# Kernel tuning notes

Hardware: AMD Instinct MI355X
Metric: run time of the kernel (lower is better)

## Reference

```python
import jax, jax.numpy as jnp
import numpy as np

LN_EPS = 1e-5

def layer_norm(x, g, b):
    mu = jnp.mean(x, axis=-1, keepdims=True)
    var = jnp.mean(jnp.square(x - mu), axis=-1, keepdims=True)
    return (x - mu) * jax.lax.rsqrt(var + LN_EPS) * g + b

def ternary_quant(w):
    # BitNet b1.58-style ternary quantization with straight-through estimator
    scale = 1.0 / jnp.clip(jnp.mean(jnp.abs(w)), 1e-5)
    wq = jnp.clip(jnp.round(w * scale), -1.0, 1.0) / scale
    return w + jax.lax.stop_gradient(wq - w)

def setup_inputs() -> dict:
    key = jax.random.key(0)
    ks = jax.random.split(key, 3)
    dim, hidden = 1024, 4096
    B, S = 8, 1024
    x = jax.random.normal(ks[0], (B, S, dim), dtype=jnp.float32)
    w1 = jax.random.normal(ks[1], (hidden, dim), dtype=jnp.float32) * 0.02
    w2 = jax.random.normal(ks[2], (dim, hidden), dtype=jnp.float32) * 0.02
    return {
        "x": x,
        "ln1_g": jnp.ones((dim,), jnp.float32), "ln1_b": jnp.zeros((dim,), jnp.float32),
        "w1": w1, "b1": jnp.zeros((hidden,), jnp.float32),
        "ln2_g": jnp.ones((hidden,), jnp.float32), "ln2_b": jnp.zeros((hidden,), jnp.float32),
        "w2": w2, "b2": jnp.zeros((dim,), jnp.float32),
    }

def reference(x, ln1_g, ln1_b, w1, b1, ln2_g, ln2_b, w2, b2):
    h = layer_norm(x, ln1_g, ln1_b)
    h = jnp.einsum('bsd,hd->bsh', h, ternary_quant(w1)) + b1  # [B,S,hidden]
    h = jax.nn.gelu(h, approximate=False)  # nn.GELU default is exact erf
    h = layer_norm(h, ln2_g, ln2_b)
    out = jnp.einsum('bsh,dh->bsd', h, ternary_quant(w2)) + b2  # [B,S,dim]
    return out
```

## Files before the change

### kernel.cpp

```cpp
#include <hip/hip_runtime.h>
#include <cstdint>
#include <cstddef>

#define DIM   1024
#define HID   4096
#define MROWS 8192

typedef __attribute__((ext_vector_type(8))) __bf16 bf16x8;
typedef __attribute__((ext_vector_type(4))) float  f32x4;
typedef __attribute__((ext_vector_type(4))) int    i32x4;

__device__ __forceinline__ unsigned short f2bf(float f) {
  unsigned int u = __float_as_uint(f);
  u += 0x7fffu + ((u >> 16) & 1u);
  return (unsigned short)(u >> 16);
}
__device__ __forceinline__ float bf2f(unsigned int lo16) {
  return __uint_as_float(lo16 << 16);
}

__device__ __forceinline__ float fast_gelu(float v) {
  float u = v * (0.79788456080286536f + 0.035677408136300125f * v * v);
  float e = __builtin_amdgcn_exp2f(u * 2.8853900817779268f);
  float r = __builtin_amdgcn_rcpf(e + 1.0f);
  return v - v * r;
}

__device__ __forceinline__ void gld16(const void* g, void* l) {
  auto* gp = reinterpret_cast<__attribute__((address_space(1))) unsigned int*>(
      reinterpret_cast<uintptr_t>(g));
  auto* lp = reinterpret_cast<__attribute__((address_space(3))) unsigned int*>(
      reinterpret_cast<uintptr_t>(l));
  __builtin_amdgcn_global_load_lds(gp, lp, 16, 0, 0);
}

__device__ __forceinline__ void wave_reduce2(float& a, float& b) {
#pragma unroll
  for (int off = 32; off > 0; off >>= 1) {
    a += __shfl_xor(a, off, 64);
    b += __shfl_xor(b, off, 64);
  }
}
__device__ __forceinline__ float wave_reduce_max(float m) {
#pragma unroll
  for (int off = 32; off > 0; off >>= 1) m = fmaxf(m, __shfl_xor(m, off, 64));
  return m;
}

__device__ __forceinline__ void block_reduce2(float& a, float& b, int tid) {
  __shared__ float red[8];
  __syncthreads();
  wave_reduce2(a, b);
  if ((tid & 63) == 0) { red[tid >> 6] = a; red[4 + (tid >> 6)] = b; }
  __syncthreads();
  a = red[0] + red[1] + red[2] + red[3];
  b = red[4] + red[5] + red[6] + red[7];
}

__global__ __launch_bounds__(256)
void prep_kernel(const float* __restrict__ w1, const float* __restrict__ w2,
                 float* __restrict__ part,
                 const float* __restrict__ x, const float* __restrict__ g,
                 const float* __restrict__ b, unsigned int* __restrict__ xn8,
                 float* __restrict__ invs) {
  int tid = threadIdx.x;
  int bid = blockIdx.x;
  if (bid < 2048) {
    const float* w = (bid < 1024) ? w1 : w2;
    int blk = bid & 1023;
    const float4* base = (const float4*)w + (size_t)blk * 1024;
    float s = 0.f;
#pragma unroll
    for (int i = 0; i < 4; ++i) {
      float4 v = base[tid + i * 256];
      s += fabsf(v.x) + fabsf(v.y) + fabsf(v.z) + fabsf(v.w);
    }
#pragma unroll
    for (int off = 32; off > 0; off >>= 1) s += __shfl_xor(s, off, 64);
    __shared__ float red[4];
    if ((tid & 63) == 0) red[tid >> 6] = s;
    __syncthreads();
    if (tid == 0) part[bid] = red[0] + red[1] + red[2] + red[3];
  } else {
    const int row  = (bid - 2048) * 4 + (tid >> 6);
    const int lane = tid & 63;
    const float4* xr = (const float4*)(x + (size_t)row * DIM);
    const float4* g4 = (const float4*)g;
    const float4* b4 = (const float4*)b;
    float4 v[4];
    float s = 0.f, ss = 0.f;
#pragma unroll
    for (int p = 0; p < 4; ++p) {
      v[p] = xr[lane + 64 * p];
      s  += v[p].x + v[p].y + v[p].z + v[p].w;
      ss += v[p].x * v[p].x + v[p].y * v[p].y + v[p].z * v[p].z + v[p].w * v[p].w;
    }
    wave_reduce2(s, ss);
    float mu  = s * (1.0f / DIM);
    float var = ss * (1.0f / DIM) - mu * mu;
    float rs  = rsqrtf(var + 1e-5f);
    float n[4][4];
    float amax = 0.f;
#pragma unroll
    for (int p = 0; p < 4; ++p) {
      float4 gg = g4[lane + 64 * p];
      float4 bb = b4[lane + 64 * p];
      n[p][0] = (v[p].x - mu) * rs * gg.x + bb.x;
      n[p][1] = (v[p].y - mu) * rs * gg.y + bb.y;
      n[p][2] = (v[p].z - mu) * rs * gg.z + bb.z;
      n[p][3] = (v[p].w - mu) * rs * gg.w + bb.w;
#pragma unroll
      for (int c = 0; c < 4; ++c) amax = fmaxf(amax, fabsf(n[p][c]));
    }
    amax = wave_reduce_max(amax);
    float sc, iv;
    if (amax < 1e-20f) { sc = 0.f; iv = 0.f; }
    else               { sc = 127.0f / amax; iv = amax * (1.0f / 127.0f); }
    if (lane == 0) invs[row] = iv;
    unsigned int* dst = xn8 + (size_t)row * 256;
#pragma unroll
    for (int p = 0; p < 4; ++p) {
      unsigned r = 0;
#pragma unroll
      for (int c = 0; c < 4; ++c) {
        int q = (int)rintf(n[p][c] * sc);
        r |= ((unsigned)q & 0xffu) << (8 * c);
      }
      dst[lane + 64 * p] = r;
    }
  }
}

__global__ __launch_bounds__(256)
void quant_kernel(const float* __restrict__ part,
                  const float* __restrict__ w1, unsigned int* __restrict__ q1,
                  const float* __restrict__ w2, unsigned short* __restrict__ q2,
                  const float* __restrict__ g2, const float* __restrict__ b2,
                  const float* __restrict__ bias2,
                  float* __restrict__ Sg, float* __restrict__ Cb,
                  float* __restrict__ scal) {
  int bid = blockIdx.x, tid = threadIdx.x;
  const int lane = tid & 63;
  const float4* psrc = (const float4*)(part + ((bid < 512) ? 0 : 1024));
  float a = 0.f, dummy = 0.f;
#pragma unroll
  for (int p = 0; p < 4; ++p) {
    float4 pv = psrc[lane + 64 * p];
    a += pv.x + pv.y + pv.z + pv.w;
  }
  wave_reduce2(a, dummy);
  float mean = fmaxf(a * (1.0f / 4194304.0f), 1e-5f);
  float sc = 1.0f / mean;

  if (bid < 512) {
    if (bid == 0 && tid == 0) scal[0] = mean;
    const int n4 = 1048576;
    int i = bid * 256 + tid;
    for (; i < n4; i += 512 * 256) {
      float4 v = ((const float4*)w1)[i];
      int t0 = (int)fminf(fmaxf(rintf(v.x * sc), -1.f), 1.f);
      int t1 = (int)fminf(fmaxf(rintf(v.y * sc), -1.f), 1.f);
      int t2 = (int)fminf(fmaxf(rintf(v.z * sc), -1.f), 1.f);
      int t3 = (int)fminf(fmaxf(rintf(v.w * sc), -1.f), 1.f);
      unsigned r = ((unsigned)t0 & 0xffu) | (((unsigned)t1 & 0xffu) << 8) |
                   (((unsigned)t2 & 0xffu) << 16) | (((unsigned)t3 & 0xffu) << 24);
      q1[i] = r;
    }
  } else {
    const int d = bid - 512;
    if (d == 0 && tid == 0) scal[1] = mean;
    const float4* wr = (const float4*)(w2 + (size_t)d * HID);
    const float4* g4 = (const float4*)g2;
    const float4* b4 = (const float4*)b2;
    uint2* qr = (uint2*)(q2 + (size_t)d * HID);
    float s1 = 0.f, s2 = 0.f;
#pragma unroll
    for (int i = 0; i < 4; ++i) {
      int idx = tid + 256 * i;
      float4 wv = wr[idx], gv = g4[idx], bv = b4[idx];
      float t0 = fminf(fmaxf(rintf(wv.x * sc), -1.f), 1.f);
      float t1 = fminf(fmaxf(rintf(wv.y * sc), -1.f), 1.f);
      float t2 = fminf(fmaxf(rintf(wv.z * sc), -1.f), 1.f);
      float t3 = fminf(fmaxf(rintf(wv.w * sc), -1.f), 1.f);
      s1 += gv.x * t0 + gv.y * t1 + gv.z * t2 + gv.w * t3;
      s2 += bv.x * t0 + bv.y * t1 + bv.z * t2 + bv.w * t3;
      uint2 r;
      r.x = (unsigned)f2bf(t0 * gv.x) | ((unsigned)f2bf(t1 * gv.y) << 16);
      r.y = (unsigned)f2bf(t2 * gv.z) | ((unsigned)f2bf(t3 * gv.w) << 16);
      qr[idx] = r;
    }
    block_reduce2(s1, s2, tid);
    if (tid == 0) {
      Sg[d] = mean * s1;
      Cb[d] = mean * s2 + bias2[d];
    }
  }
}

__global__ __launch_bounds__(256)
void gemm1_i8(const unsigned char* __restrict__ A,
              const unsigned char* __restrict__ B,
              unsigned short* __restrict__ H,
              const float* __restrict__ wscale_ptr,
              const float* __restrict__ invs,
              const float* __restrict__ bias,
              float2* __restrict__ sbuf2) {
  __shared__ unsigned char sA[3][128 * 64];
  __shared__ unsigned char sB[3][128 * 64];

  const int tid  = threadIdx.x;
  const int lane = tid & 63;
  const int wave = tid >> 6;
  const int wm   = wave & 1;
  const int wn   = wave >> 1;

  const int nbx  = gridDim.x;
  const int id   = blockIdx.y * nbx + blockIdx.x;
  const int xcd  = id & 7;
  const int slot = id >> 3;
  const int bandsPerXcd = gridDim.y >> 3;
  const int band = xcd * bandsPerXcd + slot / nbx;
  const int col  = slot - (slot / nbx) * nbx;
  const int bm   = band * 128;
  const int bn   = col * 128;

  const int csw = ((tid & 3) ^ ((tid >> 3) & 3)) * 16;
  const unsigned char* Ab = A + (size_t)(bm + (tid >> 2)) * 1024 + csw;
  const unsigned char* Bb = B + (size_t)(bn + (tid >> 2)) * 1024 + csw;

  i32x4 acc[4][4] = {};

  const int rowA = (wm * 64 + (lane & 15)) * 64;
  const int rowB = (wn * 64 + (lane & 15)) * 64;
  const int kc = (((lane >> 4) ^ ((lane >> 1) & 3))) * 16;

  gld16(Ab,                  (char*)&sA[0][0] + tid * 16);
  gld16(Ab + 64 * 1024,      (char*)&sA[0][0] + 4096 + tid * 16);
  gld16(Bb,                  (char*)&sB[0][0] + tid * 16);
  gld16(Bb + 64 * 1024,      (char*)&sB[0][0] + 4096 + tid * 16);
  gld16(Ab + 64,             (char*)&sA[1][0] + tid * 16);
  gld16(Ab + 64 * 1024 + 64, (char*)&sA[1][0] + 4096 + tid * 16);
  gld16(Bb + 64,             (char*)&sB[1][0] + tid * 16);
  gld16(Bb + 64 * 1024 + 64, (char*)&sB[1][0] + 4096 + tid * 16);
  asm volatile("s_waitcnt vmcnt(4)" ::: "memory");
  __builtin_amdgcn_s_barrier();

  int cur = 0, nx2 = 2;
  for (int t = 0; t < 16; ++t) {
    const size_t kn = (t + 2 < 16) ? (size_t)(t + 2) * 64 : 0;
    char* la = (char*)&sA[0][0] + nx2 * 8192;
    char* lb = (char*)&sB[0][0] + nx2 * 8192;
    gld16(Ab + kn,             la + tid * 16);
    gld16(Ab + 64 * 1024 + kn, la + 4096 + tid * 16);
    gld16(Bb + kn,             lb + tid * 16);
    gld16(Bb + 64 * 1024 + kn, lb + 4096 + tid * 16);
    const unsigned char* a = &sA[0][0] + cur * 8192;
    const unsigned char* b = &sB[0][0] + cur * 8192;
    i32x4 af[4], bfr[4];
#pragma unroll
    for (int i = 0; i < 4; ++i) af[i]  = *(const i32x4*)(a + rowA + i * 1024 + kc);
#pragma unroll
    for (int j = 0; j < 4; ++j) bfr[j] = *(const i32x4*)(b + rowB + j * 1024 + kc);
    __builtin_amdgcn_s_setprio(1);
#pragma unroll
    for (int i = 0; i < 4; ++i)
#pragma unroll
      for (int j = 0; j < 4; ++j)
        acc[i][j] = __builtin_amdgcn_mfma_i32_16x16x64_i8(af[i], bfr[j], acc[i][j], 0, 0, 0);
    __builtin_amdgcn_s_setprio(0);
    asm volatile("s_waitcnt vmcnt(4)" ::: "memory");
    __builtin_amdgcn_s_barrier();
    cur = (cur == 2) ? 0 : cur + 1;
    nx2 = (nx2 == 2) ? 0 : nx2 + 1;
  }
  asm volatile("s_waitcnt vmcnt(0)" ::: "memory");

  const float wscale = *wscale_ptr;
  float bv[4];
#pragma unroll
  for (int j = 0; j < 4; ++j) bv[j] = bias[bn + wn * 64 + j * 16 + (lane & 15)];
#pragma unroll
  for (int i = 0; i < 4; ++i) {
    const int m0 = bm + wm * 64 + i * 16 + ((lane >> 4) << 2);
    float asc[4];
#pragma unroll
    for (int r = 0; r < 4; ++r) asc[r] = wscale * invs[m0 + r];
#pragma unroll
    for (int r = 0; r < 4; ++r) {
      float s = 0.f, ss = 0.f;
#pragma unroll
      for (int j = 0; j < 4; ++j) {
        const int n = bn + wn * 64 + j * 16 + (lane & 15);
        float v = fast_gelu((float)acc[i][j][r] * asc[r] + bv[j]);
        H[(size_t)(m0 + r) * HID + n] = f2bf(v);
        s += v; ss += v * v;
      }
#pragma unroll
      for (int off = 1; off < 16; off <<= 1) {
        s  += __shfl_xor(s, off, 64);
        ss += __shfl_xor(ss, off, 64);
      }
      if ((lane & 15) == 0) {
        sbuf2[((size_t)(m0 + r) << 6) + (col << 1) + wn] = make_float2(s, ss);
      }
    }
  }
}

__global__ __launch_bounds__(256)
void murs_fin(const float2* __restrict__ sbuf2, const float* __restrict__ meanp,
              float2* __restrict__ murs) {
  const int row  = blockIdx.x * 4 + (threadIdx.x >> 6);
  const int lane = threadIdx.x & 63;
  float2 v = sbuf2[((size_t)row << 6) + lane];
  float s = v.x, ss = v.y;
  wave_reduce2(s, ss);
  if (lane == 0) {
    float mu  = s * (1.0f / HID);
    float var = ss * (1.0f / HID) - mu * mu;
    float rs  = rsqrtf(var + 1e-5f);
    murs[row] = make_float2(rs * meanp[1], -rs * mu);
  }
}

__global__ __launch_bounds__(512, 2)
void gemm2_v5(const unsigned short* __restrict__ A,
              const unsigned short* __restrict__ B,
              float* __restrict__ C,
              const float2* __restrict__ murs,
              const float* __restrict__ Sg,
              const float* __restrict__ Cb) {
  __shared__ unsigned short sA[3][256 * 64];
  __shared__ unsigned short sB[3][128 * 64];

  const int tid  = threadIdx.x;
  const int lane = tid & 63;
  const int wave = tid >> 6;
  const int wm   = wave >> 1;
  const int wn   = wave & 1;

  const int id   = blockIdx.y * 8 + blockIdx.x;
  const int xcd  = id & 7;
  const int slot = id >> 3;
  const int band = xcd * 4 + (slot >> 3);
  const int col  = slot & 7;
  const int bm   = band * 256;
  const int bn   = col * 128;

  const int csw = ((tid & 7) ^ ((tid >> 3) & 7)) << 3;
  const unsigned short* Ab = A + (size_t)(bm + (tid >> 3)) * 4096 + csw;
  const unsigned short* Bb = B + (size_t)(bn + (tid >> 3)) * 4096 + csw;

  const int rowAb = (wm * 64 + (lane & 15)) * 128;
  const int rowBb = (wn * 64 + (lane & 15)) * 128;
  const int hi    = lane >> 4;
  const int ck0   = ((hi)     ^ (lane & 7)) << 4;
  const int ck1   = ((hi + 4) ^ (lane & 7)) << 4;

  f32x4 acc[4][4] = {};

#pragma unroll
  for (int i = 0; i < 4; ++i) gld16(Ab + (size_t)i * 262144,      (char*)&sA[0][0] + i * 8192 + tid * 16);
#pragma unroll
  for (int i = 0; i < 2; ++i) gld16(Bb + (size_t)i * 262144,      (char*)&sB[0][0] + i * 8192 + tid * 16);
#pragma unroll
  for (int i = 0; i < 4; ++i) gld16(Ab + (size_t)i * 262144 + 64, (char*)&sA[1][0] + i * 8192 + tid * 16);
#pragma unroll
  for (int i = 0; i < 2; ++i) gld16(Bb + (size_t)i * 262144 + 64, (char*)&sB[1][0] + i * 8192 + tid * 16);
  asm volatile("s_waitcnt vmcnt(6)" ::: "memory");
  __builtin_amdgcn_s_barrier();

  int cur = 0, nx2 = 2;
  for (int t = 0; t < 64; ++t) {
    const size_t kn = (t + 2 < 64) ? (size_t)(t + 2) * 64 : 0;
    char* la = (char*)&sA[0][0] + nx2 * 32768;
    char* lb = (char*)&sB[0][0] + nx2 * 16384;
#pragma unroll
    for (int i = 0; i < 4; ++i) gld16(Ab + (size_t)i * 262144 + kn, la + i * 8192 + tid * 16);
#pragma unroll
    for (int i = 0; i < 2; ++i) gld16(Bb + (size_t)i * 262144 + kn, lb + i * 8192 + tid * 16);
    const char* a = (const char*)&sA[0][0] + cur * 32768;
    const char* b = (const char*)&sB[0][0] + cur * 16384;
    bf16x8 af[4][2], bfr[4][2];
#pragma unroll
    for (int i = 0; i < 4; ++i) {
      af[i][0] = *(const bf16x8*)(a + rowAb + i * 2048 + ck0);
      af[i][1] = *(const bf16x8*)(a + rowAb + i * 2048 + ck1);
    }
#pragma unroll
    for (int j = 0; j < 4; ++j) {
      bfr[j][0] = *(const bf16x8*)(b + rowBb + j * 2048 + ck0);
      bfr[j][1] = *(const bf16x8*)(b + rowBb + j * 2048 + ck1);
    }
    __builtin_amdgcn_s_setprio(1);
#pragma unroll
    for (int i = 0; i < 4; ++i)
#pragma unroll
      for (int j = 0; j < 4; ++j)
        acc[i][j] = __builtin_amdgcn_mfma_f32_16x16x32_bf16(af[i][0], bfr[j][0], acc[i][j], 0, 0, 0);
#pragma unroll
    for (int i = 0; i < 4; ++i)
#pragma unroll
      for (int j = 0; j < 4; ++j)
        acc[i][j] = __builtin_amdgcn_mfma_f32_16x16x32_bf16(af[i][1], bfr[j][1], acc[i][j], 0, 0, 0);
    __builtin_amdgcn_s_setprio(0);
    asm volatile("s_waitcnt vmcnt(6)" ::: "memory");
    __builtin_amdgcn_s_barrier();
    cur = (cur == 2) ? 0 : cur + 1;
    nx2 = (nx2 == 2) ? 0 : nx2 + 1;
  }
  asm volatile("s_waitcnt vmcnt(0)" ::: "memory");

  float sg[4], cb[4];
#pragma unroll
  for (int j = 0; j < 4; ++j) {
    const int n = bn + wn * 64 + j * 16 + (lane & 15);
    sg[j] = Sg[n];
    cb[j] = Cb[n];
  }
#pragma unroll
  for (int i = 0; i < 4; ++i) {
    const int m0 = bm + wm * 64 + i * 16 + (hi << 2);
#pragma unroll
    for (int r = 0; r < 4; ++r) {
      float2 ab = murs[m0 + r];
#pragma unroll
      for (int j = 0; j < 4; ++j) {
        const int n = bn + wn * 64 + j * 16 + (lane & 15);
        C[(size_t)(m0 + r) * 1024 + n] = ab.x * acc[i][j][r] + ab.y * sg[j] + cb[j];
      }
    }
  }
}

extern "C" void kernel_launch(void* const* d_in, const int* in_sizes, int n_in,
                              void* d_out, int out_size, void* d_ws, size_t ws_size,
                              hipStream_t stream) {
  const float* x     = (const float*)d_in[0];
  const float* g1    = (const float*)d_in[1];
  const float* b1v   = (const float*)d_in[2];
  const float* w1    = (const float*)d_in[3];
  const float* bias1 = (const float*)d_in[4];
  const float* g2    = (const float*)d_in[5];
  const float* b2v   = (const float*)d_in[6];
  const float* w2    = (const float*)d_in[7];
  const float* bias2 = (const float*)d_in[8];
  float* out = (float*)d_out;

  char* ws = (char*)d_ws;
  float* scal          = (float*)ws;
  float* part          = (float*)(ws + 64);
  float* invs          = (float*)(ws + 16384);
  unsigned int* q1     = (unsigned int*)(ws + 65536);
  unsigned short* q2   = (unsigned short*)(ws + 65536 + 4194304);
  unsigned int* xn8    = (unsigned int*)((char*)q2 + 8388608);
  unsigned short* h    = (unsigned short*)((char*)xn8 + 8388608);
  float2* murs         = (float2*)((char*)h + 67108864);
  float* Sg            = (float*)(murs + 8192);
  float* Cb            = Sg + 1024;
  float2* sbuf2        = (float2*)(Cb + 1024);

  prep_kernel<<<4096, 256, 0, stream>>>(w1, w2, part, x, g1, b1v, xn8, invs);
  quant_kernel<<<1536, 256, 0, stream>>>(part, w1, q1, w2, q2, g2, b2v, bias2, Sg, Cb, scal);
  gemm1_i8<<<dim3(HID / 128, MROWS / 128), 256, 0, stream>>>(
      (const unsigned char*)xn8, (const unsigned char*)q1, h, scal + 0, invs, bias1, sbuf2);
  murs_fin<<<MROWS / 4, 256, 0, stream>>>(sbuf2, scal, murs);
  gemm2_v5<<<dim3(8, 32), 512, 0, stream>>>(h, q2, out, murs, Sg, Cb);
}
```

Measured before the change: 242.5 us.

## Quantize GELU output to int8 per 64-wide segment and run GEMM2 on int8 MFMA

The first GEMM's epilogue now folds ln2 gamma into the GELU output, quantizes it to int8 with a per-row, per-64-column absmax scale, and stores those scales. The second weight is stored as packed ternary int8, using a K ordering that matches the packed activations. GEMM2 becomes an int8 MFMA kernel that rescales each 64-wide K-tile partial into float accumulators. This halves the bytes of the hidden activation written and read, and uses the faster int8 matrix path. In exchange it adds per-tile convert and FMA work in the inner loop, and activation quantization error that could affect accuracy.

```diff
diff --git a/kernel.cpp b/kernel.cpp
--- a/kernel.cpp
+++ b/kernel.cpp
@@ -14,9 +14,6 @@
   unsigned int u = __float_as_uint(f);
   u += 0x7fffu + ((u >> 16) & 1u);
   return (unsigned short)(u >> 16);
-}
-__device__ __forceinline__ float bf2f(unsigned int lo16) {
-  return __uint_as_float(lo16 << 16);
 }
 
 __device__ __forceinline__ float fast_gelu(float v) {
@@ -134,7 +131,7 @@
 __global__ __launch_bounds__(256)
 void quant_kernel(const float* __restrict__ part,
                   const float* __restrict__ w1, unsigned int* __restrict__ q1,
-                  const float* __restrict__ w2, unsigned short* __restrict__ q2,
+                  const float* __restrict__ w2, unsigned int* __restrict__ q2t,
                   const float* __restrict__ g2, const float* __restrict__ b2,
                   const float* __restrict__ bias2,
                   float* __restrict__ Sg, float* __restrict__ Cb,
@@ -169,25 +166,22 @@
   } else {
     const int d = bid - 512;
     if (d == 0 && tid == 0) scal[1] = mean;
-    const float4* wr = (const float4*)(w2 + (size_t)d * HID);
-    const float4* g4 = (const float4*)g2;
-    const float4* b4 = (const float4*)b2;
-    uint2* qr = (uint2*)(q2 + (size_t)d * HID);
+    const float* wr = w2 + (size_t)d * HID;
     float s1 = 0.f, s2 = 0.f;
 #pragma unroll
     for (int i = 0; i < 4; ++i) {
-      int idx = tid + 256 * i;
-      float4 wv = wr[idx], gv = g4[idx], bv = b4[idx];
-      float t0 = fminf(fmaxf(rintf(wv.x * sc), -1.f), 1.f);
-      float t1 = fminf(fmaxf(rintf(wv.y * sc), -1.f), 1.f);
-      float t2 = fminf(fmaxf(rintf(wv.z * sc), -1.f), 1.f);
-      float t3 = fminf(fmaxf(rintf(wv.w * sc), -1.f), 1.f);
-      s1 += gv.x * t0 + gv.y * t1 + gv.z * t2 + gv.w * t3;
-      s2 += bv.x * t0 + bv.y * t1 + bv.z * t2 + bv.w * t3;
-      uint2 r;
-      r.x = (unsigned)f2bf(t0 * gv.x) | ((unsigned)f2bf(t1 * gv.y) << 16);
-      r.y = (unsigned)f2bf(t2 * gv.z) | ((unsigned)f2bf(t3 * gv.w) << 16);
-      qr[idx] = r;
+      const int p32 = tid + 256 * i;
+      const int kb  = (p32 >> 4) * 64 + (p32 & 15);
+      unsigned r = 0;
+#pragma unroll
+      for (int j = 0; j < 4; ++j) {
+        const int k = kb + j * 16;
+        float t = fminf(fmaxf(rintf(wr[k] * sc), -1.f), 1.f);
+        s1 += g2[k] * t;
+        s2 += b2[k] * t;
+        r |= ((unsigned)(int)t & 0xffu) << (8 * j);
+      }
+      q2t[(size_t)d * 1024 + p32] = r;
     }
     block_reduce2(s1, s2, tid);
     if (tid == 0) {
@@ -200,10 +194,12 @@
 __global__ __launch_bounds__(256)
 void gemm1_i8(const unsigned char* __restrict__ A,
               const unsigned char* __restrict__ B,
-              unsigned short* __restrict__ H,
+              unsigned int* __restrict__ H8,
               const float* __restrict__ wscale_ptr,
               const float* __restrict__ invs,
               const float* __restrict__ bias,
+              const float* __restrict__ g2,
+              float* __restrict__ invsHseg,
               float2* __restrict__ sbuf2) {
   __shared__ unsigned char sA[3][128 * 64];
   __shared__ unsigned char sB[3][128 * 64];
@@ -276,9 +272,13 @@
   asm volatile("s_waitcnt vmcnt(0)" ::: "memory");
 
   const float wscale = *wscale_ptr;
-  float bv[4];
-#pragma unroll
-  for (int j = 0; j < 4; ++j) bv[j] = bias[bn + wn * 64 + j * 16 + (lane & 15)];
+  float bv[4], g2v[4];
+#pragma unroll
+  for (int j = 0; j < 4; ++j) {
+    const int n = bn + wn * 64 + j * 16 + (lane & 15);
+    bv[j]  = bias[n];
+    g2v[j] = g2[n];
+  }
 #pragma unroll
   for (int i = 0; i < 4; ++i) {
     const int m0 = bm + wm * 64 + i * 16 + ((lane >> 4) << 2);
@@ -287,20 +287,32 @@
     for (int r = 0; r < 4; ++r) asc[r] = wscale * invs[m0 + r];
 #pragma unroll
     for (int r = 0; r < 4; ++r) {
-      float s = 0.f, ss = 0.f;
+      float vg[4];
+      float s = 0.f, ss = 0.f, am = 0.f;
 #pragma unroll
       for (int j = 0; j < 4; ++j) {
-        const int n = bn + wn * 64 + j * 16 + (lane & 15);
         float v = fast_gelu((float)acc[i][j][r] * asc[r] + bv[j]);
-        H[(size_t)(m0 + r) * HID + n] = f2bf(v);
         s += v; ss += v * v;
+        vg[j] = v * g2v[j];
+        am = fmaxf(am, fabsf(vg[j]));
       }
 #pragma unroll
       for (int off = 1; off < 16; off <<= 1) {
         s  += __shfl_xor(s, off, 64);
         ss += __shfl_xor(ss, off, 64);
-      }
+        am  = fmaxf(am, __shfl_xor(am, off, 64));
+      }
+      const float qs = (am > 1e-30f) ? (127.0f / am) : 0.f;
+      unsigned pk = 0;
+#pragma unroll
+      for (int j = 0; j < 4; ++j) {
+        int q = (int)rintf(vg[j] * qs);
+        q = (q > 127) ? 127 : ((q < -127) ? -127 : q);
+        pk |= ((unsigned)q & 0xffu) << (8 * j);
+      }
+      H8[(size_t)(m0 + r) * 1024 + (bn >> 2) + wn * 16 + (lane & 15)] = pk;
       if ((lane & 15) == 0) {
+        invsHseg[(size_t)(m0 + r) * 64 + (bn >> 6) + wn] = am * (1.0f / 127.0f);
         sbuf2[((size_t)(m0 + r) << 6) + (col << 1) + wn] = make_float2(s, ss);
       }
     }
@@ -323,88 +335,96 @@
   }
 }
 
-__global__ __launch_bounds__(512, 2)
-void gemm2_v5(const unsigned short* __restrict__ A,
-              const unsigned short* __restrict__ B,
+__global__ __launch_bounds__(256)
+void gemm2_i8(const unsigned char* __restrict__ A,
+              const unsigned char* __restrict__ B,
               float* __restrict__ C,
+              const float* __restrict__ invsHseg,
               const float2* __restrict__ murs,
               const float* __restrict__ Sg,
               const float* __restrict__ Cb) {
-  __shared__ unsigned short sA[3][256 * 64];
-  __shared__ unsigned short sB[3][128 * 64];
+  __shared__ unsigned char sA[3][128 * 64];
+  __shared__ unsigned char sB[3][128 * 64];
+  __shared__ float sScL[64][128];
 
   const int tid  = threadIdx.x;
   const int lane = tid & 63;
   const int wave = tid >> 6;
-  const int wm   = wave >> 1;
-  const int wn   = wave & 1;
-
-  const int id   = blockIdx.y * 8 + blockIdx.x;
+  const int wm   = wave & 1;
+  const int wn   = wave >> 1;
+
+  const int nbx  = gridDim.x;
+  const int id   = blockIdx.y * nbx + blockIdx.x;
   const int xcd  = id & 7;
   const int slot = id >> 3;
-  const int band = xcd * 4 + (slot >> 3);
-  const int col  = slot & 7;
-  const int bm   = band * 256;
+  const int bandsPerXcd = gridDim.y >> 3;
+  const int band = xcd * bandsPerXcd + slot / nbx;
+  const int col  = slot - (slot / nbx) * nbx;
+  const int bm   = band * 128;
   const int bn   = col * 128;
 
-  const int csw = ((tid & 7) ^ ((tid >> 3) & 7)) << 3;
-  const unsigned short* Ab = A + (size_t)(bm + (tid >> 3)) * 4096 + csw;
-  const unsigned short* Bb = B + (size_t)(bn + (tid >> 3)) * 4096 + csw;
-
-  const int rowAb = (wm * 64 + (lane & 15)) * 128;
-  const int rowBb = (wn * 64 + (lane & 15)) * 128;
-  const int hi    = lane >> 4;
-  const int ck0   = ((hi)     ^ (lane & 7)) << 4;
-  const int ck1   = ((hi + 4) ^ (lane & 7)) << 4;
-
-  f32x4 acc[4][4] = {};
-
-#pragma unroll
-  for (int i = 0; i < 4; ++i) gld16(Ab + (size_t)i * 262144,      (char*)&sA[0][0] + i * 8192 + tid * 16);
-#pragma unroll
-  for (int i = 0; i < 2; ++i) gld16(Bb + (size_t)i * 262144,      (char*)&sB[0][0] + i * 8192 + tid * 16);
-#pragma unroll
-  for (int i = 0; i < 4; ++i) gld16(Ab + (size_t)i * 262144 + 64, (char*)&sA[1][0] + i * 8192 + tid * 16);
-#pragma unroll
-  for (int i = 0; i < 2; ++i) gld16(Bb + (size_t)i * 262144 + 64, (char*)&sB[1][0] + i * 8192 + tid * 16);
-  asm volatile("s_waitcnt vmcnt(6)" ::: "memory");
+  const int csw = ((tid & 3) ^ ((tid >> 3) & 3)) * 16;
+  const unsigned char* Ab = A + (size_t)(bm + (tid >> 2)) * 4096 + csw;
+  const unsigned char* Bb = B + (size_t)(bn + (tid >> 2)) * 4096 + csw;
+
+  const int rowA = (wm * 64 + (lane & 15)) * 64;
+  const int rowB = (wn * 64 + (lane & 15)) * 64;
+  const int kc = (((lane >> 4) ^ ((lane >> 1) & 3))) * 16;
+  const int hi = lane >> 4;
+
+  const float* scg = invsHseg + (size_t)bm * 64;
+  for (int u = tid; u < 8192; u += 256) {
+    sScL[u & 63][u >> 6] = scg[u];
+  }
+
+  f32x4 facc[4][4] = {};
+  const i32x4 zr = {0, 0, 0, 0};
+
+  gld16(Ab,                  (char*)&sA[0][0] + tid * 16);
+  gld16(Ab + 64 * 4096,      (char*)&sA[0][0] + 4096 + tid * 16);
+  gld16(Bb,                  (char*)&sB[0][0] + tid * 16);
+  gld16(Bb + 64 * 4096,      (char*)&sB[0][0] + 4096 + tid * 16);
+  gld16(Ab + 64,             (char*)&sA[1][0] + tid * 16);
+  gld16(Ab + 64 * 4096 + 64, (char*)&sA[1][0] + 4096 + tid * 16);
+  gld16(Bb + 64,             (char*)&sB[1][0] + tid * 16);
+  gld16(Bb + 64 * 4096 + 64, (char*)&sB[1][0] + 4096 + tid * 16);
+  asm volatile("s_waitcnt vmcnt(4)" ::: "memory");
   __builtin_amdgcn_s_barrier();
 
   int cur = 0, nx2 = 2;
   for (int t = 0; t < 64; ++t) {
     const size_t kn = (t + 2 < 64) ? (size_t)(t + 2) * 64 : 0;
-    char* la = (char*)&sA[0][0] + nx2 * 32768;
-    char* lb = (char*)&sB[0][0] + nx2 * 16384;
-#pragma unroll
-    for (int i = 0; i < 4; ++i) gld16(Ab + (size_t)i * 262144 + kn, la + i * 8192 + tid * 16);
-#pragma unroll
-    for (int i = 0; i < 2; ++i) gld16(Bb + (size_t)i * 262144 + kn, lb + i * 8192 + tid * 16);
-    const char* a = (const char*)&sA[0][0] + cur * 32768;
-    const char* b = (const char*)&sB[0][0] + cur * 16384;
-    bf16x8 af[4][2], bfr[4][2];
-#pragma unroll
-    for (int i = 0; i < 4; ++i) {
-      af[i][0] = *(const bf16x8*)(a + rowAb + i * 2048 + ck0);
-      af[i][1] = *(const bf16x8*)(a + rowAb + i * 2048 + ck1);
-    }
-#pragma unroll
-    for (int j = 0; j < 4; ++j) {
-      bfr[j][0] = *(const bf16x8*)(b + rowBb + j * 2048 + ck0);
-      bfr[j][1] = *(const bf16x8*)(b + rowBb + j * 2048 + ck1);
-    }
+    char* la = (char*)&sA[0][0] + nx2 * 8192;
+    char* lb = (char*)&sB[0][0] + nx2 * 8192;
+    gld16(Ab + kn,             la + tid * 16);
+    gld16(Ab + 64 * 4096 + kn, la + 4096 + tid * 16);
+    gld16(Bb + kn,             lb + tid * 16);
+    gld16(Bb + 64 * 4096 + kn, lb + 4096 + tid * 16);
+    const unsigned char* a = &sA[0][0] + cur * 8192;
+    const unsigned char* b = &sB[0][0] + cur * 8192;
+    i32x4 af[4], bfr[4];
+#pragma unroll
+    for (int i = 0; i < 4; ++i) af[i]  = *(const i32x4*)(a + rowA + i * 1024 + kc);
+#pragma unroll
+    for (int j = 0; j < 4; ++j) bfr[j] = *(const i32x4*)(b + rowB + j * 1024 + kc);
+    float scl[4][4];
+#pragma unroll
+    for (int i = 0; i < 4; ++i)
+#pragma unroll
+      for (int r = 0; r < 4; ++r)
+        scl[i][r] = sScL[t][wm * 64 + i * 16 + hi * 4 + r];
     __builtin_amdgcn_s_setprio(1);
 #pragma unroll
     for (int i = 0; i < 4; ++i)
 #pragma unroll
-      for (int j = 0; j < 4; ++j)
-        acc[i][j] = __builtin_amdgcn_mfma_f32_16x16x32_bf16(af[i][0], bfr[j][0], acc[i][j], 0, 0, 0);
-#pragma unroll
-    for (int i = 0; i < 4; ++i)
-#pragma unroll
-      for (int j = 0; j < 4; ++j)
-        acc[i][j] = __builtin_amdgcn_mfma_f32_16x16x32_bf16(af[i][1], bfr[j][1], acc[i][j], 0, 0, 0);
+      for (int j = 0; j < 4; ++j) {
+        i32x4 ia = __builtin_amdgcn_mfma_i32_16x16x64_i8(af[i], bfr[j], zr, 0, 0, 0);
+#pragma unroll
+        for (int r = 0; r < 4; ++r)
+          facc[i][j][r] += (float)ia[r] * scl[i][r];
+      }
     __builtin_amdgcn_s_setprio(0);
-    asm volatile("s_waitcnt vmcnt(6)" ::: "memory");
+    asm volatile("s_waitcnt vmcnt(4)" ::: "memory");
     __builtin_amdgcn_s_barrier();
     cur = (cur == 2) ? 0 : cur + 1;
     nx2 = (nx2 == 2) ? 0 : nx2 + 1;
@@ -427,7 +447,7 @@
 #pragma unroll
       for (int j = 0; j < 4; ++j) {
         const int n = bn + wn * 64 + j * 16 + (lane & 15);
-        C[(size_t)(m0 + r) * 1024 + n] = ab.x * acc[i][j][r] + ab.y * sg[j] + cb[j];
+        C[(size_t)(m0 + r) * 1024 + n] = ab.x * facc[i][j][r] + ab.y * sg[j] + cb[j];
       }
     }
   }
@@ -452,18 +472,21 @@
   float* part          = (float*)(ws + 64);
   float* invs          = (float*)(ws + 16384);
   unsigned int* q1     = (unsigned int*)(ws + 65536);
-  unsigned short* q2   = (unsigned short*)(ws + 65536 + 4194304);
-  unsigned int* xn8    = (unsigned int*)((char*)q2 + 8388608);
-  unsigned short* h    = (unsigned short*)((char*)xn8 + 8388608);
-  float2* murs         = (float2*)((char*)h + 67108864);
+  unsigned int* q2t    = (unsigned int*)(ws + 65536 + 4194304);
+  unsigned int* xn8    = (unsigned int*)((char*)q2t + 4194304);
+  unsigned int* H8     = (unsigned int*)((char*)xn8 + 8388608);
+  float* invsHseg      = (float*)((char*)H8 + 33554432);
+  float2* murs         = (float2*)((char*)invsHseg + 2097152);
   float* Sg            = (float*)(murs + 8192);
   float* Cb            = Sg + 1024;
   float2* sbuf2        = (float2*)(Cb + 1024);
 
   prep_kernel<<<4096, 256, 0, stream>>>(w1, w2, part, x, g1, b1v, xn8, invs);
-  quant_kernel<<<1536, 256, 0, stream>>>(part, w1, q1, w2, q2, g2, b2v, bias2, Sg, Cb, scal);
+  quant_kernel<<<1536, 256, 0, stream>>>(part, w1, q1, w2, q2t, g2, b2v, bias2, Sg, Cb, scal);
   gemm1_i8<<<dim3(HID / 128, MROWS / 128), 256, 0, stream>>>(
-      (const unsigned char*)xn8, (const unsigned char*)q1, h, scal + 0, invs, bias1, sbuf2);
+      (const unsigned char*)xn8, (const unsigned char*)q1, H8, scal + 0, invs, bias1,
+      g2, invsHseg, sbuf2);
   murs_fin<<<MROWS / 4, 256, 0, stream>>>(sbuf2, scal, murs);
-  gemm2_v5<<<dim3(8, 32), 512, 0, stream>>>(h, q2, out, murs, Sg, Cb);
-}
+  gemm2_i8<<<dim3(DIM / 128, MROWS / 128), 256, 0, stream>>>(
+      (const unsigned char*)H8, (const unsigned char*)q2t, out, invsHseg, murs, Sg, Cb);
+}
```

Result: slower. 265.8 us (+9.6%).

## Enlarge gemm1 block tile to 256x128 with doubled per-wave M work

Applied to the files above, without the earlier changes.

The int8 GEMM1 block tile grows from 128x128 to 256x128, so each wave now computes 128x64 with 32 accumulators, and the grid halves along M. This raises the amount of B-fragment reuse per LDS load and cuts global traffic for the weight matrix. In exchange it needs more registers and LDS per block (launch_bounds 256,2), so occupancy drops, and with fewer blocks the work may fill the CUs less evenly. An unused bf16 helper is also removed.

```diff
diff --git a/kernel.cpp b/kernel.cpp
--- a/kernel.cpp
+++ b/kernel.cpp
@@ -14,9 +14,6 @@
   unsigned int u = __float_as_uint(f);
   u += 0x7fffu + ((u >> 16) & 1u);
   return (unsigned short)(u >> 16);
-}
-__device__ __forceinline__ float bf2f(unsigned int lo16) {
-  return __uint_as_float(lo16 << 16);
 }
 
 __device__ __forceinline__ float fast_gelu(float v) {
@@ -197,7 +194,7 @@
   }
 }
 
-__global__ __launch_bounds__(256)
+__global__ __launch_bounds__(256, 2)
 void gemm1_i8(const unsigned char* __restrict__ A,
               const unsigned char* __restrict__ B,
               unsigned short* __restrict__ H,
@@ -205,7 +202,7 @@
               const float* __restrict__ invs,
               const float* __restrict__ bias,
               float2* __restrict__ sbuf2) {
-  __shared__ unsigned char sA[3][128 * 64];
+  __shared__ unsigned char sA[3][256 * 64];
   __shared__ unsigned char sB[3][128 * 64];
 
   const int tid  = threadIdx.x;
@@ -221,58 +218,67 @@
   const int bandsPerXcd = gridDim.y >> 3;
   const int band = xcd * bandsPerXcd + slot / nbx;
   const int col  = slot - (slot / nbx) * nbx;
-  const int bm   = band * 128;
+  const int bm   = band * 256;
   const int bn   = col * 128;
 
   const int csw = ((tid & 3) ^ ((tid >> 3) & 3)) * 16;
   const unsigned char* Ab = A + (size_t)(bm + (tid >> 2)) * 1024 + csw;
   const unsigned char* Bb = B + (size_t)(bn + (tid >> 2)) * 1024 + csw;
 
-  i32x4 acc[4][4] = {};
-
-  const int rowA = (wm * 64 + (lane & 15)) * 64;
-  const int rowB = (wn * 64 + (lane & 15)) * 64;
+  i32x4 acc[8][4] = {};
+
+  const int rowA = (wm * 128 + (lane & 15)) * 64;
+  const int rowB = (wn * 64  + (lane & 15)) * 64;
   const int kc = (((lane >> 4) ^ ((lane >> 1) & 3))) * 16;
-
-  gld16(Ab,                  (char*)&sA[0][0] + tid * 16);
-  gld16(Ab + 64 * 1024,      (char*)&sA[0][0] + 4096 + tid * 16);
-  gld16(Bb,                  (char*)&sB[0][0] + tid * 16);
-  gld16(Bb + 64 * 1024,      (char*)&sB[0][0] + 4096 + tid * 16);
-  gld16(Ab + 64,             (char*)&sA[1][0] + tid * 16);
-  gld16(Ab + 64 * 1024 + 64, (char*)&sA[1][0] + 4096 + tid * 16);
-  gld16(Bb + 64,             (char*)&sB[1][0] + tid * 16);
-  gld16(Bb + 64 * 1024 + 64, (char*)&sB[1][0] + 4096 + tid * 16);
-  asm volatile("s_waitcnt vmcnt(4)" ::: "memory");
+  const int hi = lane >> 4;
+
+#define STAGE1(BUF, K0)                                                     \
+  do {                                                                      \
+    char* la_ = (char*)&sA[0][0] + (BUF) * 16384;                           \
+    char* lb_ = (char*)&sB[0][0] + (BUF) * 8192;                            \
+    gld16(Ab + (K0),                 la_ + tid * 16);                       \
+    gld16(Ab + 64 * 1024 + (K0),     la_ + 4096 + tid * 16);                \
+    gld16(Ab + 128 * 1024 + (K0),    la_ + 8192 + tid * 16);                \
+    gld16(Ab + 192 * 1024 + (K0),    la_ + 12288 + tid * 16);               \
+    gld16(Bb + (K0),                 lb_ + tid * 16);                       \
+    gld16(Bb + 64 * 1024 + (K0),     lb_ + 4096 + tid * 16);                \
+  } while (0)
+
+  STAGE1(0, 0);
+  STAGE1(1, 64);
+  asm volatile("s_waitcnt vmcnt(6)" ::: "memory");
   __builtin_amdgcn_s_barrier();
 
   int cur = 0, nx2 = 2;
   for (int t = 0; t < 16; ++t) {
     const size_t kn = (t + 2 < 16) ? (size_t)(t + 2) * 64 : 0;
-    char* la = (char*)&sA[0][0] + nx2 * 8192;
-    char* lb = (char*)&sB[0][0] + nx2 * 8192;
-    gld16(Ab + kn,             la + tid * 16);
-    gld16(Ab + 64 * 1024 + kn, la + 4096 + tid * 16);
-    gld16(Bb + kn,             lb + tid * 16);
-    gld16(Bb + 64 * 1024 + kn, lb + 4096 + tid * 16);
-    const unsigned char* a = &sA[0][0] + cur * 8192;
+    STAGE1(nx2, kn);
+    const unsigned char* a = &sA[0][0] + cur * 16384;
     const unsigned char* b = &sB[0][0] + cur * 8192;
-    i32x4 af[4], bfr[4];
-#pragma unroll
-    for (int i = 0; i < 4; ++i) af[i]  = *(const i32x4*)(a + rowA + i * 1024 + kc);
+    i32x4 bfr[4];
 #pragma unroll
     for (int j = 0; j < 4; ++j) bfr[j] = *(const i32x4*)(b + rowB + j * 1024 + kc);
-    __builtin_amdgcn_s_setprio(1);
-#pragma unroll
-    for (int i = 0; i < 4; ++i)
-#pragma unroll
-      for (int j = 0; j < 4; ++j)
-        acc[i][j] = __builtin_amdgcn_mfma_i32_16x16x64_i8(af[i], bfr[j], acc[i][j], 0, 0, 0);
-    __builtin_amdgcn_s_setprio(0);
-    asm volatile("s_waitcnt vmcnt(4)" ::: "memory");
+#pragma unroll
+    for (int h2 = 0; h2 < 2; ++h2) {
+      i32x4 af[4];
+#pragma unroll
+      for (int i = 0; i < 4; ++i)
+        af[i] = *(const i32x4*)(a + rowA + (h2 * 4 + i) * 1024 + kc);
+      __builtin_amdgcn_s_setprio(1);
+#pragma unroll
+      for (int i = 0; i < 4; ++i)
+#pragma unroll
+        for (int j = 0; j < 4; ++j)
+          acc[h2 * 4 + i][j] =
+              __builtin_amdgcn_mfma_i32_16x16x64_i8(af[i], bfr[j], acc[h2 * 4 + i][j], 0, 0, 0);
+      __builtin_amdgcn_s_setprio(0);
+    }
+    asm volatile("s_waitcnt vmcnt(6)" ::: "memory");
     __builtin_amdgcn_s_barrier();
     cur = (cur == 2) ? 0 : cur + 1;
     nx2 = (nx2 == 2) ? 0 : nx2 + 1;
   }
+#undef STAGE1
   asm volatile("s_waitcnt vmcnt(0)" ::: "memory");
 
   const float wscale = *wscale_ptr;
@@ -280,8 +286,8 @@
 #pragma unroll
   for (int j = 0; j < 4; ++j) bv[j] = bias[bn + wn * 64 + j * 16 + (lane & 15)];
 #pragma unroll
-  for (int i = 0; i < 4; ++i) {
-    const int m0 = bm + wm * 64 + i * 16 + ((lane >> 4) << 2);
+  for (int i = 0; i < 8; ++i) {
+    const int m0 = bm + wm * 128 + i * 16 + (hi << 2);
     float asc[4];
 #pragma unroll
     for (int r = 0; r < 4; ++r) asc[r] = wscale * invs[m0 + r];
@@ -462,7 +468,7 @@
 
   prep_kernel<<<4096, 256, 0, stream>>>(w1, w2, part, x, g1, b1v, xn8, invs);
   quant_kernel<<<1536, 256, 0, stream>>>(part, w1, q1, w2, q2, g2, b2v, bias2, Sg, Cb, scal);
-  gemm1_i8<<<dim3(HID / 128, MROWS / 128), 256, 0, stream>>>(
+  gemm1_i8<<<dim3(HID / 128, MROWS / 256), 256, 0, stream>>>(
       (const unsigned char*)xn8, (const unsigned char*)q1, h, scal + 0, invs, bias1, sbuf2);
   murs_fin<<<MROWS / 4, 256, 0, stream>>>(sbuf2, scal, murs);
   gemm2_v5<<<dim3(8, 32), 512, 0, stream>>>(h, q2, out, murs, Sg, Cb);
```

New measurement: 244.1 us. About the same (+0.7%).
